# Kernel tuning notes

Measured on AMD Instinct MI355X. Metric: run time of the kernel, lower is better.

The kernel has to match this reference:

```python
import jax, jax.numpy as jnp
import numpy as np

D_MODEL = 1024
N_HEADS = 16
D_K = D_MODEL // N_HEADS
ROPE_THETA = 10000.0


def setup_inputs() -> dict:
    key = jax.random.key(0)
    ks = jax.random.split(key, 5)
    B, S = 2, 2048
    scale = 1.0 / np.sqrt(D_MODEL)
    return {
        "x": jax.random.normal(ks[0], (B, S, D_MODEL), dtype=jnp.float32),
        "token_positions": jnp.arange(S, dtype=jnp.int32),
        "Wq": jax.random.normal(ks[1], (D_MODEL, D_MODEL), dtype=jnp.float32) * scale,
        "Wk": jax.random.normal(ks[2], (D_MODEL, D_MODEL), dtype=jnp.float32) * scale,
        "Wv": jax.random.normal(ks[3], (D_MODEL, D_MODEL), dtype=jnp.float32) * scale,
        "Wo": jax.random.normal(ks[4], (D_MODEL, D_MODEL), dtype=jnp.float32) * scale,
    }


def apply_rope(x, positions):
    # x: [b, h, s, d_k]; interleaved-pair rotary embedding, theta=10000
    half = D_K // 2
    inv_freq = ROPE_THETA ** (-jnp.arange(0, half, dtype=x.dtype) * 2.0 / D_K)  # [half]
    angles = positions.astype(x.dtype)[:, None] * inv_freq[None, :]             # [s, half]
    cos, sin = jnp.cos(angles), jnp.sin(angles)                                 # [s, half]
    x1 = x[..., 0::2]
    x2 = x[..., 1::2]
    r1 = x1 * cos - x2 * sin
    r2 = x1 * sin + x2 * cos
    # re-interleave
    return jnp.stack([r1, r2], axis=-1).reshape(x.shape)


def reference(x, token_positions, Wq, Wk, Wv, Wo):
    B, S, _ = x.shape
    # Linear(d_model, d_model) with no bias: y = x @ W.T
    Q = jnp.einsum("bsd,ed->bse", x, Wq).reshape(B, S, N_HEADS, D_K).transpose(0, 2, 1, 3)
    K = jnp.einsum("bsd,ed->bse", x, Wk).reshape(B, S, N_HEADS, D_K).transpose(0, 2, 1, 3)
    V = jnp.einsum("bsd,ed->bse", x, Wv).reshape(B, S, N_HEADS, D_K).transpose(0, 2, 1, 3)
    Q = apply_rope(Q, token_positions)
    K = apply_rope(K, token_positions)
    scores = jnp.einsum("bhqd,bhkd->bhqk", Q, K) / jnp.sqrt(jnp.asarray(D_K, x.dtype))
    causal = jnp.tril(jnp.ones((S, S), dtype=bool))
    scores = jnp.where(causal[None, None, :, :], scores, jnp.asarray(-jnp.inf, x.dtype))
    attn = jax.nn.softmax(scores, axis=-1)
    out = jnp.einsum("bhqk,bhkd->bhqd", attn, V)            # [b, h, s, d_k]
    out = out.transpose(0, 2, 1, 3).reshape(B, S, D_MODEL)   # [b, s, d_model]
    return jnp.einsum("bsd,ed->bse", out, Wo)
```

## Files before the change

### kernel.cpp

```cpp
#include <hip/hip_runtime.h>
#include <math.h>

#define SEQ 2048
#define NH  16
#define DKH 64
#define DM  1024
#define MR  4096

using bf16x8 = __attribute__((ext_vector_type(8))) short;
using f32x4  = __attribute__((ext_vector_type(4))) float;

__device__ __forceinline__ ushort f2b(float f) {
  unsigned u = __float_as_uint(f);
  return (ushort)((u + 0x7fffu + ((u >> 16) & 1u)) >> 16);
}

__device__ __forceinline__ float exp2_fast(float x) {
  float r; asm("v_exp_f32 %0, %1" : "=v"(r) : "v"(x)); return r;
}

__device__ __forceinline__ unsigned cvt_pk(float lo, float hi) {
  unsigned r; asm("v_cvt_pk_bf16_f32 %0, %1, %2" : "=v"(r) : "v"(lo), "v"(hi));
  return r;
}

__device__ __forceinline__ void gll16(const void* g, void* l) {
  __builtin_amdgcn_global_load_lds(
      (const __attribute__((address_space(1))) void*)g,
      (__attribute__((address_space(3))) void*)l, 16, 0, 0);
}

__global__ __launch_bounds__(256) void cvt_all(
    const float* __restrict__ x,  const float* __restrict__ wq,
    const float* __restrict__ wk, const float* __restrict__ wv,
    const float* __restrict__ wo,
    ushort* __restrict__ xb,  ushort* __restrict__ wqb, ushort* __restrict__ wkb,
    ushort* __restrict__ wvb, ushort* __restrict__ wob)
{
  size_t e = ((size_t)blockIdx.x * 256 + threadIdx.x) * 4;
  const float* s; ushort* d; size_t off;
  if      (e < 4194304) { s = x;  d = xb;  off = e; }
  else if (e < 5242880) { s = wq; d = wqb; off = e - 4194304; }
  else if (e < 6291456) { s = wk; d = wkb; off = e - 5242880; }
  else if (e < 7340032) { s = wv; d = wvb; off = e - 6291456; }
  else                  { s = wo; d = wob; off = e - 7340032; }
  float4 f = *(const float4*)(s + off);
  ushort4 o4 = { f2b(f.x), f2b(f.y), f2b(f.z), f2b(f.w) };
  *(ushort4*)(d + off) = o4;
}

__global__ __launch_bounds__(512) void gemm_qkv(
    const ushort* __restrict__ X,
    const ushort* __restrict__ Wq, const ushort* __restrict__ Wk, const ushort* __restrict__ Wv,
    ushort* __restrict__ Q, ushort* __restrict__ K, ushort* __restrict__ Vt,
    const int* __restrict__ pos)
{
  __shared__ __align__(16) char As[2][16384];
  __shared__ __align__(16) char Bs[2][16384];

  const int id  = blockIdx.x;
  const int xcd = id & 7;
  const int i   = id >> 3;
  const int mt  = xcd * 4 + (i & 3);
  const int nt  = i >> 2;
  const int m0  = mt * 128;
  const int nG  = nt * 128;
  const int z   = nG >> 10;
  const int n0  = nG & 1023;
  const ushort* W = (z == 0) ? Wq : (z == 1) ? Wk : Wv;

  const int tid  = threadIdx.x;
  const int lane = tid & 63;
  const int w    = tid >> 6;
  const int wm   = (w >> 2) * 64;
  const int wn   = (w & 3) * 32;
  const int li   = lane & 15;
  const int g    = lane >> 4;

  f32x4 acc[4][2] = {};

  auto stage = [&](int t, int buf) {
    const int k0 = t * 64;
    #pragma unroll
    for (int it = 0; it < 2; ++it) {
      const int L  = w * 2048 + it * 1024 + lane * 16;
      const int r  = L >> 7;
      const int sc = ((L >> 4) & 7) ^ (r & 7);
      gll16(X + (size_t)(m0 + r) * DM + k0 + sc * 8, &As[buf][w * 2048 + it * 1024]);
      gll16(W + (size_t)(n0 + r) * DM + k0 + sc * 8, &Bs[buf][w * 2048 + it * 1024]);
    }
  };

  auto compute = [&](int buf) {
    #pragma unroll
    for (int ks = 0; ks < 2; ++ks) {
      bf16x8 af[4], bfr[2];
      #pragma unroll
      for (int mf = 0; mf < 4; ++mf) {
        const int row = wm + mf * 16 + li;
        af[mf] = *(const bf16x8*)(&As[buf][row * 128 + (((ks * 4 + g) ^ (row & 7)) << 4)]);
      }
      #pragma unroll
      for (int nf = 0; nf < 2; ++nf) {
        const int row = wn + nf * 16 + li;
        bfr[nf] = *(const bf16x8*)(&Bs[buf][row * 128 + (((ks * 4 + g) ^ (row & 7)) << 4)]);
      }
      #pragma unroll
      for (int mf = 0; mf < 4; ++mf)
        #pragma unroll
        for (int nf = 0; nf < 2; ++nf)
          acc[mf][nf] = __builtin_amdgcn_mfma_f32_16x16x32_bf16(af[mf], bfr[nf], acc[mf][nf], 0, 0, 0);
    }
  };

  stage(0, 0);
  for (int t = 0; t < 16; ++t) {
    if (t < 15) {
      stage(t + 1, (t + 1) & 1);
      __builtin_amdgcn_sched_barrier(0);
      asm volatile("s_waitcnt vmcnt(4)" ::: "memory");
    } else {
      asm volatile("s_waitcnt vmcnt(0)" ::: "memory");
    }
    __builtin_amdgcn_s_barrier();
    __builtin_amdgcn_sched_barrier(0);
    compute(t & 1);
    __builtin_amdgcn_sched_barrier(0);
    __builtin_amdgcn_s_barrier();
  }

  #pragma unroll
  for (int nf = 0; nf < 2; ++nf) {
    const int n = n0 + wn + nf * 16 + li;
    const int h = n >> 6;
    const int d = n & 63;
    if (z == 2) {
      #pragma unroll
      for (int mf = 0; mf < 4; ++mf) {
        const int m  = m0 + wm + mf * 16 + g * 4;
        const int b  = m >> 11;
        const int s2 = m & (SEQ - 1);
        ushort4 pk = { f2b(acc[mf][nf][0]), f2b(acc[mf][nf][1]),
                       f2b(acc[mf][nf][2]), f2b(acc[mf][nf][3]) };
        *(ushort4*)(Vt + (((size_t)b * NH + h) * DKH + d) * SEQ + s2) = pk;
      }
    } else {
      ushort* DST = (z == 0) ? Q : K;
      const float freq = __expf(-(float)(d >> 1) * 0.2878231366242557f);
      #pragma unroll
      for (int mf = 0; mf < 4; ++mf) {
        #pragma unroll
        for (int r = 0; r < 4; ++r) {
          const int m  = m0 + wm + mf * 16 + g * 4 + r;
          const int b  = m >> 11;
          const int s2 = m & (SEQ - 1);
          const float ang = (float)pos[s2] * freq;
          float sn, cs;
          __sincosf(ang, &sn, &cs);
          const float v1 = acc[mf][nf][r];
          const float v2 = __shfl_xor(v1, 1);
          float ov = (d & 1) ? (v2 * sn + v1 * cs)
                             : (v1 * cs - v2 * sn);
          if (z == 0) ov *= 0.1803368801111204f;
          DST[(((size_t)b * NH + h) * SEQ + s2) * DKH + d] = f2b(ov);
        }
      }
    }
  }
}

__global__ __launch_bounds__(512) void gemm_wo(
    const ushort* __restrict__ A, const ushort* __restrict__ W,
    float* __restrict__ out)
{
  __shared__ __align__(16) char As[2][16384];
  __shared__ __align__(16) char Bs[2][16384];

  const int id  = blockIdx.x;
  const int xcd = id & 7;
  const int i   = id >> 3;
  const int mt  = xcd * 4 + (i & 3);
  const int nt  = i >> 2;
  const int m0  = mt * 128;
  const int n0  = nt * 128;

  const int tid  = threadIdx.x;
  const int lane = tid & 63;
  const int w    = tid >> 6;
  const int wm   = (w >> 2) * 64;
  const int wn   = (w & 3) * 32;
  const int li   = lane & 15;
  const int g    = lane >> 4;

  f32x4 acc[4][2] = {};

  auto stage = [&](int t, int buf) {
    const int k0 = t * 64;
    #pragma unroll
    for (int it = 0; it < 2; ++it) {
      const int L  = w * 2048 + it * 1024 + lane * 16;
      const int r  = L >> 7;
      const int sc = ((L >> 4) & 7) ^ (r & 7);
      gll16(A + (size_t)(m0 + r) * DM + k0 + sc * 8, &As[buf][w * 2048 + it * 1024]);
      gll16(W + (size_t)(n0 + r) * DM + k0 + sc * 8, &Bs[buf][w * 2048 + it * 1024]);
    }
  };

  auto compute = [&](int buf) {
    #pragma unroll
    for (int ks = 0; ks < 2; ++ks) {
      bf16x8 af[4], bfr[2];
      #pragma unroll
      for (int mf = 0; mf < 4; ++mf) {
        const int row = wm + mf * 16 + li;
        af[mf] = *(const bf16x8*)(&As[buf][row * 128 + (((ks * 4 + g) ^ (row & 7)) << 4)]);
      }
      #pragma unroll
      for (int nf = 0; nf < 2; ++nf) {
        const int row = wn + nf * 16 + li;
        bfr[nf] = *(const bf16x8*)(&Bs[buf][row * 128 + (((ks * 4 + g) ^ (row & 7)) << 4)]);
      }
      #pragma unroll
      for (int mf = 0; mf < 4; ++mf)
        #pragma unroll
        for (int nf = 0; nf < 2; ++nf)
          acc[mf][nf] = __builtin_amdgcn_mfma_f32_16x16x32_bf16(af[mf], bfr[nf], acc[mf][nf], 0, 0, 0);
    }
  };

  stage(0, 0);
  for (int t = 0; t < 16; ++t) {
    if (t < 15) {
      stage(t + 1, (t + 1) & 1);
      __builtin_amdgcn_sched_barrier(0);
      asm volatile("s_waitcnt vmcnt(4)" ::: "memory");
    } else {
      asm volatile("s_waitcnt vmcnt(0)" ::: "memory");
    }
    __builtin_amdgcn_s_barrier();
    __builtin_amdgcn_sched_barrier(0);
    compute(t & 1);
    __builtin_amdgcn_sched_barrier(0);
    __builtin_amdgcn_s_barrier();
  }

  #pragma unroll
  for (int nf = 0; nf < 2; ++nf)
    #pragma unroll
    for (int mf = 0; mf < 4; ++mf)
      #pragma unroll
      for (int r = 0; r < 4; ++r)
        out[(size_t)(m0 + wm + mf * 16 + g * 4 + r) * DM + n0 + wn + nf * 16 + li] = acc[mf][nf][r];
}

__global__ __launch_bounds__(256) void attn(
    const ushort* __restrict__ Q, const ushort* __restrict__ K,
    const ushort* __restrict__ Vt, ushort* __restrict__ AO)
{
  __shared__ __align__(16) char KsB[2][8192];
  __shared__ __align__(16) char VsB[2][8192];
  __shared__ __align__(16) char Ps[8192];

  const int tid  = threadIdx.x;
  const int lane = tid & 63;
  const int w    = tid >> 6;
  const int li   = lane & 15;
  const int g    = lane >> 4;

  const int bx  = blockIdx.x;
  const int xcd = bx & 7;
  const int idx = bx >> 3;
  const int j   = idx >> 2;
  const int s   = idx & 3;
  const int qb  = (s & 1) ? (31 - j) : j;
  const int bh  = s * 8 + xcd;
  const int q0b = qb * 64;
  const int n   = qb + 1;
  const int q0w = q0b + w * 16;

  const ushort* Qb = Q  + (size_t)bh * SEQ * DKH;
  const ushort* Kb = K  + (size_t)bh * SEQ * DKH;
  const ushort* Vb = Vt + (size_t)bh * DKH * SEQ;
  char* Pw = Ps + w * 2048;

  const bf16x8 qf0 = *(const bf16x8*)(Qb + (size_t)(q0w + li) * DKH + g * 8);
  const bf16x8 qf1 = *(const bf16x8*)(Qb + (size_t)(q0w + li) * DKH + 32 + g * 8);

  f32x4 o[4] = {};
  float m_ = -INFINITY, l_ = 0.f;

  auto stage = [&](int kt, int buf) {
    const int k0 = kt * 64;
    #pragma unroll
    for (int it = 0; it < 2; ++it) {
      const int L  = w * 2048 + it * 1024 + lane * 16;
      const int r  = L >> 7;
      const int sc = ((L >> 4) & 7) ^ (r & 7);
      gll16(Kb + (size_t)(k0 + r) * DKH + sc * 8, &KsB[buf][w * 2048 + it * 1024]);
      gll16(Vb + (size_t)r * SEQ + k0 + sc * 8,   &VsB[buf][w * 2048 + it * 1024]);
    }
  };

  auto computeT = [&](int t, bool diag) {
    const int k0 = t * 64;
    const char* Kc = KsB[t & 1];
    const char* Vc = VsB[t & 1];

    f32x4 st[4] = {};
    __builtin_amdgcn_s_setprio(1);
    #pragma unroll
    for (int nf = 0; nf < 4; ++nf) {
      const int row = nf * 16 + li;
      bf16x8 kfa = *(const bf16x8*)(Kc + row * 128 + (((0 + g) ^ (row & 7)) << 4));
      bf16x8 kfb = *(const bf16x8*)(Kc + row * 128 + (((4 + g) ^ (row & 7)) << 4));
      st[nf] = __builtin_amdgcn_mfma_f32_16x16x32_bf16(kfa, qf0, st[nf], 0, 0, 0);
      st[nf] = __builtin_amdgcn_mfma_f32_16x16x32_bf16(kfb, qf1, st[nf], 0, 0, 0);
    }
    __builtin_amdgcn_s_setprio(0);

    if (diag) {
      #pragma unroll
      for (int nf = 0; nf < 4; ++nf)
        #pragma unroll
        for (int r = 0; r < 4; ++r)
          if (k0 + nf * 16 + g * 4 + r > q0w + li) st[nf][r] = -1e30f;
    }

    float mx = fmaxf(fmaxf(fmaxf(st[0][0], st[0][1]), fmaxf(st[0][2], st[0][3])),
                     fmaxf(fmaxf(st[1][0], st[1][1]), fmaxf(st[1][2], st[1][3])));
    mx = fmaxf(mx, fmaxf(fmaxf(fmaxf(st[2][0], st[2][1]), fmaxf(st[2][2], st[2][3])),
                         fmaxf(fmaxf(st[3][0], st[3][1]), fmaxf(st[3][2], st[3][3]))));
    mx = fmaxf(mx, __shfl_xor(mx, 16));
    mx = fmaxf(mx, __shfl_xor(mx, 32));

    const bool rescale = !__all(mx - m_ <= 8.0f);
    float al = 1.0f;
    if (rescale) {
      const float newm = fmaxf(m_, mx);
      al = exp2_fast(m_ - newm);
      m_ = newm;
    }

    float p[4][4];
    float rs = 0.f;
    #pragma unroll
    for (int nf = 0; nf < 4; ++nf)
      #pragma unroll
      for (int r = 0; r < 4; ++r) {
        p[nf][r] = exp2_fast(st[nf][r] - m_);
        rs += p[nf][r];
      }
    rs += __shfl_xor(rs, 16);
    rs += __shfl_xor(rs, 32);

    if (rescale) {
      l_ = l_ * al + rs;
      float alr[4];
      #pragma unroll
      for (int r = 0; r < 4; ++r) alr[r] = __shfl(al, g * 4 + r);
      #pragma unroll
      for (int nf = 0; nf < 4; ++nf)
        #pragma unroll
        for (int r = 0; r < 4; ++r) o[nf][r] *= alr[r];
    } else {
      l_ += rs;
    }

    #pragma unroll
    for (int nf = 0; nf < 4; ++nf) {
      uint2 pv = { cvt_pk(p[nf][0], p[nf][1]), cvt_pk(p[nf][2], p[nf][3]) };
      const int cw = nf * 2 + (g >> 1);
      *(uint2*)(Pw + li * 128 + ((cw ^ (li & 7)) << 4) + ((g & 1) << 3)) = pv;
    }
    bf16x8 pf0 = *(const bf16x8*)(Pw + li * 128 + (((0 + g) ^ (li & 7)) << 4));
    bf16x8 pf1 = *(const bf16x8*)(Pw + li * 128 + (((4 + g) ^ (li & 7)) << 4));

    __builtin_amdgcn_s_setprio(1);
    #pragma unroll
    for (int nf = 0; nf < 4; ++nf) {
      const int row = nf * 16 + li;
      bf16x8 vfa = *(const bf16x8*)(Vc + row * 128 + (((0 + g) ^ (row & 7)) << 4));
      bf16x8 vfb = *(const bf16x8*)(Vc + row * 128 + (((4 + g) ^ (row & 7)) << 4));
      o[nf] = __builtin_amdgcn_mfma_f32_16x16x32_bf16(pf0, vfa, o[nf], 0, 0, 0);
      o[nf] = __builtin_amdgcn_mfma_f32_16x16x32_bf16(pf1, vfb, o[nf], 0, 0, 0);
    }
    __builtin_amdgcn_s_setprio(0);
  };

  stage(0, 0);
  for (int t = 0; t < n; ++t) {
    if (t + 1 < n) {
      stage(t + 1, (t + 1) & 1);
      __builtin_amdgcn_sched_barrier(0);
      asm volatile("s_waitcnt vmcnt(4)" ::: "memory");
    } else {
      asm volatile("s_waitcnt vmcnt(0)" ::: "memory");
    }
    __builtin_amdgcn_s_barrier();
    __builtin_amdgcn_sched_barrier(0);
    computeT(t, t == n - 1);
    __builtin_amdgcn_sched_barrier(0);
    __builtin_amdgcn_s_barrier();
  }

  const float inv = 1.0f / l_;
  float ir[4];
  #pragma unroll
  for (int r = 0; r < 4; ++r) ir[r] = __shfl(inv, g * 4 + r);

  const int b = bh >> 4, h = bh & 15;
  #pragma unroll
  for (int nf = 0; nf < 4; ++nf)
    #pragma unroll
    for (int r = 0; r < 4; ++r) {
      const int q = q0w + g * 4 + r;
      AO[((size_t)b * SEQ + q) * DM + h * DKH + nf * 16 + li] = f2b(o[nf][r] * ir[r]);
    }
}

extern "C" void kernel_launch(void* const* d_in, const int* in_sizes, int n_in,
                              void* d_out, int out_size, void* d_ws, size_t ws_size,
                              hipStream_t stream)
{
  const float* x   = (const float*)d_in[0];
  const int*   pos = (const int*)  d_in[1];
  const float* Wq  = (const float*)d_in[2];
  const float* Wk  = (const float*)d_in[3];
  const float* Wv  = (const float*)d_in[4];
  const float* Wo  = (const float*)d_in[5];
  float* out = (float*)d_out;

  ushort* ws  = (ushort*)d_ws;
  ushort* xb  = ws;
  ushort* wqb = xb  + 4194304;
  ushort* wkb = wqb + 1048576;
  ushort* wvb = wkb + 1048576;
  ushort* wob = wvb + 1048576;
  ushort* Qb  = wob + 1048576;
  ushort* Kb  = Qb  + 4194304;
  ushort* Vtb = Kb  + 4194304;
  ushort* AOb = Vtb + 4194304;

  cvt_all<<<8192, 256, 0, stream>>>(x, Wq, Wk, Wv, Wo, xb, wqb, wkb, wvb, wob);
  gemm_qkv<<<768, 512, 0, stream>>>(xb, wqb, wkb, wvb, Qb, Kb, Vtb, pos);
  attn<<<1024, 256, 0, stream>>>(Qb, Kb, Vtb, AOb);
  gemm_wo<<<256, 512, 0, stream>>>(AOb, wob, out);
}
```

Measured before the change: 113.6 us.

## Pair complementary causal query blocks per workgroup and stage 128-key tiles

Each attention workgroup now processes two query blocks (p and 31-p) in sequence, so every block does a balanced amount of causal work and the grid halves to 512. K/V staging moves to 128-key chunks double-buffered in larger LDS buffers, giving two 64-key compute steps per barrier pair. This aims to remove load imbalance and tail effects from the triangular work and to cut sync overhead per key. In exchange it uses twice the LDS per block, which may lower occupancy, and it serializes the two segments within one workgroup.

```diff
diff --git a/kernel.cpp b/kernel.cpp
--- a/kernel.cpp
+++ b/kernel.cpp
@@ -257,8 +257,8 @@
     const ushort* __restrict__ Q, const ushort* __restrict__ K,
     const ushort* __restrict__ Vt, ushort* __restrict__ AO)
 {
-  __shared__ __align__(16) char KsB[2][8192];
-  __shared__ __align__(16) char VsB[2][8192];
+  __shared__ __align__(16) char KsB[2][16384];
+  __shared__ __align__(16) char VsB[2][16384];
   __shared__ __align__(16) char Ps[8192];
 
   const int tid  = threadIdx.x;
@@ -270,41 +270,59 @@
   const int bx  = blockIdx.x;
   const int xcd = bx & 7;
   const int idx = bx >> 3;
-  const int j   = idx >> 2;
+  const int p   = idx >> 2;
   const int s   = idx & 3;
-  const int qb  = (s & 1) ? (31 - j) : j;
   const int bh  = s * 8 + xcd;
-  const int q0b = qb * 64;
-  const int n   = qb + 1;
-  const int q0w = q0b + w * 16;
+  const int segA = 31 - p;
+  const int segB = p;
+  const int ncA = (segA + 2) >> 1;
+  const int ncB = (segB + 2) >> 1;
+  const int nT  = ncA + ncB;
 
   const ushort* Qb = Q  + (size_t)bh * SEQ * DKH;
   const ushort* Kb = K  + (size_t)bh * SEQ * DKH;
   const ushort* Vb = Vt + (size_t)bh * DKH * SEQ;
   char* Pw = Ps + w * 2048;
-
-  const bf16x8 qf0 = *(const bf16x8*)(Qb + (size_t)(q0w + li) * DKH + g * 8);
-  const bf16x8 qf1 = *(const bf16x8*)(Qb + (size_t)(q0w + li) * DKH + 32 + g * 8);
+  const int b = bh >> 4, h = bh & 15;
+
+  const int qA = segA * 64 + w * 16;
+  const int qB = segB * 64 + w * 16;
+  const bf16x8 qfA0 = *(const bf16x8*)(Qb + (size_t)(qA + li) * DKH + g * 8);
+  const bf16x8 qfA1 = *(const bf16x8*)(Qb + (size_t)(qA + li) * DKH + 32 + g * 8);
+  const bf16x8 qfB0 = *(const bf16x8*)(Qb + (size_t)(qB + li) * DKH + g * 8);
+  const bf16x8 qfB1 = *(const bf16x8*)(Qb + (size_t)(qB + li) * DKH + 32 + g * 8);
 
   f32x4 o[4] = {};
   float m_ = -INFINITY, l_ = 0.f;
-
-  auto stage = [&](int kt, int buf) {
-    const int k0 = kt * 64;
-    #pragma unroll
-    for (int it = 0; it < 2; ++it) {
-      const int L  = w * 2048 + it * 1024 + lane * 16;
+  bf16x8 qf0 = qfA0, qf1 = qfA1;
+  int seg = segA, q0w = qA;
+
+  auto stage = [&](int i, int buf) {
+    const int c  = (i < ncA) ? i : i - ncA;
+    const int k0 = c * 128;
+    #pragma unroll
+    for (int it = 0; it < 4; ++it) {
+      const int L  = w * 4096 + it * 1024 + lane * 16;
       const int r  = L >> 7;
-      const int sc = ((L >> 4) & 7) ^ (r & 7);
-      gll16(Kb + (size_t)(k0 + r) * DKH + sc * 8, &KsB[buf][w * 2048 + it * 1024]);
-      gll16(Vb + (size_t)r * SEQ + k0 + sc * 8,   &VsB[buf][w * 2048 + it * 1024]);
-    }
-  };
-
-  auto computeT = [&](int t, bool diag) {
+      const int c3 = ((L >> 4) & 7) ^ (r & 7);
+      gll16(Kb + (size_t)(k0 + r) * DKH + c3 * 8, &KsB[buf][w * 4096 + it * 1024]);
+    }
+    #pragma unroll
+    for (int it = 0; it < 4; ++it) {
+      const int L  = w * 4096 + it * 1024 + lane * 16;
+      const int r  = L >> 8;
+      const int lb = L & 255;
+      const int j  = lb >> 7;
+      const int c3 = ((lb >> 4) & 7) ^ (r & 7);
+      gll16(Vb + (size_t)r * SEQ + k0 + j * 64 + c3 * 8, &VsB[buf][w * 4096 + it * 1024]);
+    }
+  };
+
+  auto computeT = [&](int t, int j, int buf) {
     const int k0 = t * 64;
-    const char* Kc = KsB[t & 1];
-    const char* Vc = VsB[t & 1];
+    const char* Kc = &KsB[buf][j * 8192];
+    const char* Vc = &VsB[buf][0];
+    const int vjo = j * 128;
 
     f32x4 st[4] = {};
     __builtin_amdgcn_s_setprio(1);
@@ -318,7 +336,7 @@
     }
     __builtin_amdgcn_s_setprio(0);
 
-    if (diag) {
+    if (t == seg) {
       #pragma unroll
       for (int nf = 0; nf < 4; ++nf)
         #pragma unroll
@@ -341,14 +359,14 @@
       m_ = newm;
     }
 
-    float p[4][4];
+    float pv[4][4];
     float rs = 0.f;
     #pragma unroll
     for (int nf = 0; nf < 4; ++nf)
       #pragma unroll
       for (int r = 0; r < 4; ++r) {
-        p[nf][r] = exp2_fast(st[nf][r] - m_);
-        rs += p[nf][r];
+        pv[nf][r] = exp2_fast(st[nf][r] - m_);
+        rs += pv[nf][r];
       }
     rs += __shfl_xor(rs, 16);
     rs += __shfl_xor(rs, 32);
@@ -368,9 +386,9 @@
 
     #pragma unroll
     for (int nf = 0; nf < 4; ++nf) {
-      uint2 pv = { cvt_pk(p[nf][0], p[nf][1]), cvt_pk(p[nf][2], p[nf][3]) };
+      uint2 pk = { cvt_pk(pv[nf][0], pv[nf][1]), cvt_pk(pv[nf][2], pv[nf][3]) };
       const int cw = nf * 2 + (g >> 1);
-      *(uint2*)(Pw + li * 128 + ((cw ^ (li & 7)) << 4) + ((g & 1) << 3)) = pv;
+      *(uint2*)(Pw + li * 128 + ((cw ^ (li & 7)) << 4) + ((g & 1) << 3)) = pk;
     }
     bf16x8 pf0 = *(const bf16x8*)(Pw + li * 128 + (((0 + g) ^ (li & 7)) << 4));
     bf16x8 pf1 = *(const bf16x8*)(Pw + li * 128 + (((4 + g) ^ (li & 7)) << 4));
@@ -379,43 +397,60 @@
     #pragma unroll
     for (int nf = 0; nf < 4; ++nf) {
       const int row = nf * 16 + li;
-      bf16x8 vfa = *(const bf16x8*)(Vc + row * 128 + (((0 + g) ^ (row & 7)) << 4));
-      bf16x8 vfb = *(const bf16x8*)(Vc + row * 128 + (((4 + g) ^ (row & 7)) << 4));
+      bf16x8 vfa = *(const bf16x8*)(Vc + row * 256 + vjo + (((0 + g) ^ (row & 7)) << 4));
+      bf16x8 vfb = *(const bf16x8*)(Vc + row * 256 + vjo + (((4 + g) ^ (row & 7)) << 4));
       o[nf] = __builtin_amdgcn_mfma_f32_16x16x32_bf16(pf0, vfa, o[nf], 0, 0, 0);
       o[nf] = __builtin_amdgcn_mfma_f32_16x16x32_bf16(pf1, vfb, o[nf], 0, 0, 0);
     }
     __builtin_amdgcn_s_setprio(0);
   };
 
+  auto finalize = [&]() {
+    const float inv = 1.0f / l_;
+    float ir[4];
+    #pragma unroll
+    for (int r = 0; r < 4; ++r) ir[r] = __shfl(inv, g * 4 + r);
+    #pragma unroll
+    for (int nf = 0; nf < 4; ++nf)
+      #pragma unroll
+      for (int r = 0; r < 4; ++r) {
+        const int q = q0w + g * 4 + r;
+        AO[((size_t)b * SEQ + q) * DM + h * DKH + nf * 16 + li] = f2b(o[nf][r] * ir[r]);
+      }
+  };
+
   stage(0, 0);
-  for (int t = 0; t < n; ++t) {
-    if (t + 1 < n) {
-      stage(t + 1, (t + 1) & 1);
+  for (int i = 0; i < nT; ++i) {
+    if (i + 1 < nT) {
+      stage(i + 1, (i + 1) & 1);
       __builtin_amdgcn_sched_barrier(0);
-      asm volatile("s_waitcnt vmcnt(4)" ::: "memory");
+      asm volatile("s_waitcnt vmcnt(8)" ::: "memory");
     } else {
       asm volatile("s_waitcnt vmcnt(0)" ::: "memory");
     }
     __builtin_amdgcn_s_barrier();
     __builtin_amdgcn_sched_barrier(0);
-    computeT(t, t == n - 1);
-    __builtin_amdgcn_sched_barrier(0);
-    __builtin_amdgcn_s_barrier();
+
+    const int c = (i < ncA) ? i : i - ncA;
+    #pragma unroll
+    for (int j = 0; j < 2; ++j) {
+      const int t = 2 * c + j;
+      if (t <= seg) computeT(t, j, i & 1);
+    }
+
+    __builtin_amdgcn_sched_barrier(0);
+    __builtin_amdgcn_s_barrier();
+
+    if (i == ncA - 1) {
+      finalize();
+      #pragma unroll
+      for (int nf = 0; nf < 4; ++nf) o[nf] = f32x4{0.f, 0.f, 0.f, 0.f};
+      m_ = -INFINITY; l_ = 0.f;
+      qf0 = qfB0; qf1 = qfB1;
+      seg = segB; q0w = qB;
+    }
   }
-
-  const float inv = 1.0f / l_;
-  float ir[4];
-  #pragma unroll
-  for (int r = 0; r < 4; ++r) ir[r] = __shfl(inv, g * 4 + r);
-
-  const int b = bh >> 4, h = bh & 15;
-  #pragma unroll
-  for (int nf = 0; nf < 4; ++nf)
-    #pragma unroll
-    for (int r = 0; r < 4; ++r) {
-      const int q = q0w + g * 4 + r;
-      AO[((size_t)b * SEQ + q) * DM + h * DKH + nf * 16 + li] = f2b(o[nf][r] * ir[r]);
-    }
+  finalize();
 }
 
 extern "C" void kernel_launch(void* const* d_in, const int* in_sizes, int n_in,
@@ -443,6 +478,6 @@
 
   cvt_all<<<8192, 256, 0, stream>>>(x, Wq, Wk, Wv, Wo, xb, wqb, wkb, wvb, wob);
   gemm_qkv<<<768, 512, 0, stream>>>(xb, wqb, wkb, wvb, Qb, Kb, Vtb, pos);
-  attn<<<1024, 256, 0, stream>>>(Qb, Kb, Vtb, AOb);
+  attn<<<512, 256, 0, stream>>>(Qb, Kb, Vtb, AOb);
   gemm_wo<<<256, 512, 0, stream>>>(AOb, wob, out);
 }
```

Result: faster. 108.4 us (-4.5%).

## Rewrite attention with 32x32 MFMA, 128-query blocks and register-resident P

Applied to the files above, without the earlier changes.

The attention kernel now gives each block 128 queries, with 32 per wave, and uses 32x32x16 bf16 MFMAs for both QK^T and PV. The P tile is passed to the PV MFMA through permlane32_swap instead of a round trip through shared memory, and the row max and row sum reductions also use permlane swaps. This removes the LDS write/read of P and its shared buffer, halves the grid, and reuses each K/V tile across more queries. In exchange each block does more work, which costs occupancy and load balance. Waves near the diagonal sit idle on some tiles, and the larger f32x16 accumulators raise register pressure.

```diff
diff --git a/kernel.cpp b/kernel.cpp
--- a/kernel.cpp
+++ b/kernel.cpp
@@ -1,4 +1,5 @@
 #include <hip/hip_runtime.h>
+#include <hip/hip_bf16.h>
 #include <math.h>
 
 #define SEQ 2048
@@ -9,6 +10,7 @@
 
 using bf16x8 = __attribute__((ext_vector_type(8))) short;
 using f32x4  = __attribute__((ext_vector_type(4))) float;
+using f32x16 = __attribute__((ext_vector_type(16))) float;
 
 __device__ __forceinline__ ushort f2b(float f) {
   unsigned u = __float_as_uint(f);
@@ -20,8 +22,17 @@
 }
 
 __device__ __forceinline__ unsigned cvt_pk(float lo, float hi) {
-  unsigned r; asm("v_cvt_pk_bf16_f32 %0, %1, %2" : "=v"(r) : "v"(lo), "v"(hi));
-  return r;
+  __hip_bfloat162 h = __float22bfloat162_rn(float2{lo, hi});
+  return *reinterpret_cast<unsigned*>(&h);
+}
+
+__device__ __forceinline__ float xhalf_max(float x) {
+  auto r = __builtin_amdgcn_permlane32_swap(__float_as_uint(x), __float_as_uint(x), false, false);
+  return fmaxf(__uint_as_float(r[0]), __uint_as_float(r[1]));
+}
+__device__ __forceinline__ float xhalf_add(float x) {
+  auto r = __builtin_amdgcn_permlane32_swap(__float_as_uint(x), __float_as_uint(x), false, false);
+  return __uint_as_float(r[0]) + __uint_as_float(r[1]);
 }
 
 __device__ __forceinline__ void gll16(const void* g, void* l) {
@@ -259,34 +270,35 @@
 {
   __shared__ __align__(16) char KsB[2][8192];
   __shared__ __align__(16) char VsB[2][8192];
-  __shared__ __align__(16) char Ps[8192];
 
   const int tid  = threadIdx.x;
   const int lane = tid & 63;
   const int w    = tid >> 6;
-  const int li   = lane & 15;
-  const int g    = lane >> 4;
+  const int lq   = lane & 31;
+  const int hi   = lane >> 5;
 
   const int bx  = blockIdx.x;
   const int xcd = bx & 7;
   const int idx = bx >> 3;
-  const int j   = idx >> 2;
-  const int s   = idx & 3;
-  const int qb  = (s & 1) ? (31 - j) : j;
-  const int bh  = s * 8 + xcd;
-  const int q0b = qb * 64;
-  const int n   = qb + 1;
-  const int q0w = q0b + w * 16;
+  int u, s;
+  if (idx < 32) { u = 15 - (idx >> 1); s = idx & 1; }
+  else          { u = (idx - 32) >> 1; s = 2 + ((idx - 32) & 1); }
+  const int bh   = s * 8 + xcd;
+  const int ntr  = 2 * u + 2;
+  const int q0w  = u * 128 + w * 32;
+  const int q_abs = q0w + lq;
+  const int t_max = (q0w + 31) >> 6;
 
   const ushort* Qb = Q  + (size_t)bh * SEQ * DKH;
   const ushort* Kb = K  + (size_t)bh * SEQ * DKH;
   const ushort* Vb = Vt + (size_t)bh * DKH * SEQ;
-  char* Pw = Ps + w * 2048;
-
-  const bf16x8 qf0 = *(const bf16x8*)(Qb + (size_t)(q0w + li) * DKH + g * 8);
-  const bf16x8 qf1 = *(const bf16x8*)(Qb + (size_t)(q0w + li) * DKH + 32 + g * 8);
-
-  f32x4 o[4] = {};
+
+  bf16x8 qf[4];
+  #pragma unroll
+  for (int db = 0; db < 4; ++db)
+    qf[db] = *(const bf16x8*)(Qb + (size_t)(q0w + lq) * DKH + db * 16 + hi * 8);
+
+  f32x16 o0 = {}, o1 = {};
   float m_ = -INFINITY, l_ = 0.f;
 
   auto stage = [&](int kt, int buf) {
@@ -301,95 +313,85 @@
     }
   };
 
-  auto computeT = [&](int t, bool diag) {
+#define PVSTEP(P, S4) do {                                                   \
+    unsigned A0 = cvt_pk((P)[((S4)&1)*8 + 0], (P)[((S4)&1)*8 + 1]);          \
+    unsigned A1 = cvt_pk((P)[((S4)&1)*8 + 2], (P)[((S4)&1)*8 + 3]);          \
+    unsigned B0 = cvt_pk((P)[((S4)&1)*8 + 4], (P)[((S4)&1)*8 + 5]);          \
+    unsigned B1 = cvt_pk((P)[((S4)&1)*8 + 6], (P)[((S4)&1)*8 + 7]);          \
+    auto r0 = __builtin_amdgcn_permlane32_swap(A0, B0, false, false);        \
+    auto r1 = __builtin_amdgcn_permlane32_swap(A1, B1, false, false);        \
+    int4 ti = { (int)r0[0], (int)r1[0], (int)r0[1], (int)r1[1] };            \
+    bf16x8 pf = *(bf16x8*)&ti;                                               \
+    const int uv = (S4) * 2 + hi;                                            \
+    bf16x8 va = *(const bf16x8*)(Vc + lq * 128      + ((uv ^ (lq & 7)) << 4)); \
+    bf16x8 vb = *(const bf16x8*)(Vc + (32+lq) * 128 + ((uv ^ (lq & 7)) << 4)); \
+    o0 = __builtin_amdgcn_mfma_f32_32x32x16_bf16(va, pf, o0, 0, 0, 0);       \
+    o1 = __builtin_amdgcn_mfma_f32_32x32x16_bf16(vb, pf, o1, 0, 0, 0);       \
+  } while (0)
+
+  auto computeT = [&](int t, int buf, bool diag) {
+    const char* Kc = KsB[buf];
+    const char* Vc = VsB[buf];
     const int k0 = t * 64;
-    const char* Kc = KsB[t & 1];
-    const char* Vc = VsB[t & 1];
-
-    f32x4 st[4] = {};
+
+    f32x16 st0 = {}, st1 = {};
     __builtin_amdgcn_s_setprio(1);
     #pragma unroll
-    for (int nf = 0; nf < 4; ++nf) {
-      const int row = nf * 16 + li;
-      bf16x8 kfa = *(const bf16x8*)(Kc + row * 128 + (((0 + g) ^ (row & 7)) << 4));
-      bf16x8 kfb = *(const bf16x8*)(Kc + row * 128 + (((4 + g) ^ (row & 7)) << 4));
-      st[nf] = __builtin_amdgcn_mfma_f32_16x16x32_bf16(kfa, qf0, st[nf], 0, 0, 0);
-      st[nf] = __builtin_amdgcn_mfma_f32_16x16x32_bf16(kfb, qf1, st[nf], 0, 0, 0);
+    for (int db = 0; db < 4; ++db) {
+      const int uk = db * 2 + hi;
+      bf16x8 ka = *(const bf16x8*)(Kc + lq * 128      + ((uk ^ (lq & 7)) << 4));
+      bf16x8 kb = *(const bf16x8*)(Kc + (32+lq) * 128 + ((uk ^ (lq & 7)) << 4));
+      st0 = __builtin_amdgcn_mfma_f32_32x32x16_bf16(ka, qf[db], st0, 0, 0, 0);
+      st1 = __builtin_amdgcn_mfma_f32_32x32x16_bf16(kb, qf[db], st1, 0, 0, 0);
     }
     __builtin_amdgcn_s_setprio(0);
 
     if (diag) {
       #pragma unroll
-      for (int nf = 0; nf < 4; ++nf)
-        #pragma unroll
-        for (int r = 0; r < 4; ++r)
-          if (k0 + nf * 16 + g * 4 + r > q0w + li) st[nf][r] = -1e30f;
-    }
-
-    float mx = fmaxf(fmaxf(fmaxf(st[0][0], st[0][1]), fmaxf(st[0][2], st[0][3])),
-                     fmaxf(fmaxf(st[1][0], st[1][1]), fmaxf(st[1][2], st[1][3])));
-    mx = fmaxf(mx, fmaxf(fmaxf(fmaxf(st[2][0], st[2][1]), fmaxf(st[2][2], st[2][3])),
-                         fmaxf(fmaxf(st[3][0], st[3][1]), fmaxf(st[3][2], st[3][3]))));
-    mx = fmaxf(mx, __shfl_xor(mx, 16));
-    mx = fmaxf(mx, __shfl_xor(mx, 32));
-
-    const bool rescale = !__all(mx - m_ <= 8.0f);
+      for (int reg = 0; reg < 16; ++reg) {
+        const int kvr = (reg & 3) + 8 * (reg >> 2) + 4 * hi;
+        if (k0 + kvr > q_abs)      st0[reg] = -1e30f;
+        if (k0 + 32 + kvr > q_abs) st1[reg] = -1e30f;
+      }
+    }
+
+    float mx = st0[0];
+    #pragma unroll
+    for (int r = 1; r < 16; ++r) mx = fmaxf(mx, st0[r]);
+    #pragma unroll
+    for (int r = 0; r < 16; ++r) mx = fmaxf(mx, st1[r]);
+    mx = xhalf_max(mx);
+
+    const bool resc = !__all(mx - m_ <= 8.0f);
     float al = 1.0f;
-    if (rescale) {
-      const float newm = fmaxf(m_, mx);
-      al = exp2_fast(m_ - newm);
-      m_ = newm;
-    }
-
-    float p[4][4];
+    if (resc) { const float nm = fmaxf(m_, mx); al = exp2_fast(m_ - nm); m_ = nm; }
+
     float rs = 0.f;
     #pragma unroll
-    for (int nf = 0; nf < 4; ++nf)
-      #pragma unroll
-      for (int r = 0; r < 4; ++r) {
-        p[nf][r] = exp2_fast(st[nf][r] - m_);
-        rs += p[nf][r];
-      }
-    rs += __shfl_xor(rs, 16);
-    rs += __shfl_xor(rs, 32);
-
-    if (rescale) {
+    for (int r = 0; r < 16; ++r) { st0[r] = exp2_fast(st0[r] - m_); rs += st0[r]; }
+    #pragma unroll
+    for (int r = 0; r < 16; ++r) { st1[r] = exp2_fast(st1[r] - m_); rs += st1[r]; }
+    rs = xhalf_add(rs);
+
+    if (resc) {
       l_ = l_ * al + rs;
-      float alr[4];
-      #pragma unroll
-      for (int r = 0; r < 4; ++r) alr[r] = __shfl(al, g * 4 + r);
-      #pragma unroll
-      for (int nf = 0; nf < 4; ++nf)
-        #pragma unroll
-        for (int r = 0; r < 4; ++r) o[nf][r] *= alr[r];
+      #pragma unroll
+      for (int r = 0; r < 16; ++r) { o0[r] *= al; o1[r] *= al; }
     } else {
       l_ += rs;
     }
 
-    #pragma unroll
-    for (int nf = 0; nf < 4; ++nf) {
-      uint2 pv = { cvt_pk(p[nf][0], p[nf][1]), cvt_pk(p[nf][2], p[nf][3]) };
-      const int cw = nf * 2 + (g >> 1);
-      *(uint2*)(Pw + li * 128 + ((cw ^ (li & 7)) << 4) + ((g & 1) << 3)) = pv;
-    }
-    bf16x8 pf0 = *(const bf16x8*)(Pw + li * 128 + (((0 + g) ^ (li & 7)) << 4));
-    bf16x8 pf1 = *(const bf16x8*)(Pw + li * 128 + (((4 + g) ^ (li & 7)) << 4));
-
     __builtin_amdgcn_s_setprio(1);
-    #pragma unroll
-    for (int nf = 0; nf < 4; ++nf) {
-      const int row = nf * 16 + li;
-      bf16x8 vfa = *(const bf16x8*)(Vc + row * 128 + (((0 + g) ^ (row & 7)) << 4));
-      bf16x8 vfb = *(const bf16x8*)(Vc + row * 128 + (((4 + g) ^ (row & 7)) << 4));
-      o[nf] = __builtin_amdgcn_mfma_f32_16x16x32_bf16(pf0, vfa, o[nf], 0, 0, 0);
-      o[nf] = __builtin_amdgcn_mfma_f32_16x16x32_bf16(pf1, vfb, o[nf], 0, 0, 0);
-    }
+    PVSTEP(st0, 0);
+    PVSTEP(st0, 1);
+    PVSTEP(st1, 2);
+    PVSTEP(st1, 3);
     __builtin_amdgcn_s_setprio(0);
   };
 
   stage(0, 0);
-  for (int t = 0; t < n; ++t) {
-    if (t + 1 < n) {
+  for (int t = 0; t < ntr; ++t) {
+    if (t + 1 < ntr) {
       stage(t + 1, (t + 1) & 1);
       __builtin_amdgcn_sched_barrier(0);
       asm volatile("s_waitcnt vmcnt(4)" ::: "memory");
@@ -398,24 +400,27 @@
     }
     __builtin_amdgcn_s_barrier();
     __builtin_amdgcn_sched_barrier(0);
-    computeT(t, t == n - 1);
+    if (t <= t_max) computeT(t, t & 1, t == t_max);
     __builtin_amdgcn_sched_barrier(0);
     __builtin_amdgcn_s_barrier();
   }
 
   const float inv = 1.0f / l_;
-  float ir[4];
-  #pragma unroll
-  for (int r = 0; r < 4; ++r) ir[r] = __shfl(inv, g * 4 + r);
-
   const int b = bh >> 4, h = bh & 15;
-  #pragma unroll
-  for (int nf = 0; nf < 4; ++nf)
-    #pragma unroll
-    for (int r = 0; r < 4; ++r) {
-      const int q = q0w + g * 4 + r;
-      AO[((size_t)b * SEQ + q) * DM + h * DKH + nf * 16 + li] = f2b(o[nf][r] * ir[r]);
-    }
+  ushort* dst = AO + ((size_t)b * SEQ + q_abs) * DM + h * DKH;
+
+#define STORE16(OV, DSUB) do {                                               \
+    _Pragma("unroll")                                                        \
+    for (int rq = 0; rq < 4; ++rq) {                                         \
+      const int d0 = (DSUB) * 32 + rq * 8 + hi * 4;                          \
+      uint2 pk = { cvt_pk((OV)[rq*4+0] * inv, (OV)[rq*4+1] * inv),           \
+                   cvt_pk((OV)[rq*4+2] * inv, (OV)[rq*4+3] * inv) };         \
+      *(uint2*)(dst + d0) = pk;                                              \
+    }                                                                        \
+  } while (0)
+
+  STORE16(o0, 0);
+  STORE16(o1, 1);
 }
 
 extern "C" void kernel_launch(void* const* d_in, const int* in_sizes, int n_in,
@@ -443,6 +448,6 @@
 
   cvt_all<<<8192, 256, 0, stream>>>(x, Wq, Wk, Wv, Wo, xb, wqb, wkb, wvb, wob);
   gemm_qkv<<<768, 512, 0, stream>>>(xb, wqb, wkb, wvb, Qb, Kb, Vtb, pos);
-  attn<<<1024, 256, 0, stream>>>(Qb, Kb, Vtb, AOb);
+  attn<<<512, 256, 0, stream>>>(Qb, Kb, Vtb, AOb);
   gemm_wo<<<256, 512, 0, stream>>>(AOb, wob, out);
 }
```

Result: slower. 118.0 us (+3.8%).

## Drop K/V double buffering in attention and use HIP bf16 pack intrinsic

Applied to the files above, without the earlier changes.

Replaces the double-buffered K/V LDS staging in the attention kernel with a single buffer. Each tile is now loaded and then waited on with __syncthreads before compute, instead of prefetching the next tile with manual vmcnt waits. This cuts LDS use per block from 40KB to 24KB, which may let more blocks share a CU, but global-load latency is no longer overlapped with MFMA work. The inline-asm bf16 pack is also swapped for the __float22bfloat162_rn intrinsic.

```diff
diff --git a/kernel.cpp b/kernel.cpp
--- a/kernel.cpp
+++ b/kernel.cpp
@@ -1,4 +1,5 @@
 #include <hip/hip_runtime.h>
+#include <hip/hip_bf16.h>
 #include <math.h>
 
 #define SEQ 2048
@@ -20,8 +21,8 @@
 }
 
 __device__ __forceinline__ unsigned cvt_pk(float lo, float hi) {
-  unsigned r; asm("v_cvt_pk_bf16_f32 %0, %1, %2" : "=v"(r) : "v"(lo), "v"(hi));
-  return r;
+  __hip_bfloat162 h = __float22bfloat162_rn(float2{lo, hi});
+  return *reinterpret_cast<unsigned*>(&h);
 }
 
 __device__ __forceinline__ void gll16(const void* g, void* l) {
@@ -257,8 +258,8 @@
     const ushort* __restrict__ Q, const ushort* __restrict__ K,
     const ushort* __restrict__ Vt, ushort* __restrict__ AO)
 {
-  __shared__ __align__(16) char KsB[2][8192];
-  __shared__ __align__(16) char VsB[2][8192];
+  __shared__ __align__(16) char Ks[8192];
+  __shared__ __align__(16) char Vs[8192];
   __shared__ __align__(16) char Ps[8192];
 
   const int tid  = threadIdx.x;
@@ -289,30 +290,28 @@
   f32x4 o[4] = {};
   float m_ = -INFINITY, l_ = 0.f;
 
-  auto stage = [&](int kt, int buf) {
+  auto stage = [&](int kt) {
     const int k0 = kt * 64;
     #pragma unroll
     for (int it = 0; it < 2; ++it) {
       const int L  = w * 2048 + it * 1024 + lane * 16;
       const int r  = L >> 7;
       const int sc = ((L >> 4) & 7) ^ (r & 7);
-      gll16(Kb + (size_t)(k0 + r) * DKH + sc * 8, &KsB[buf][w * 2048 + it * 1024]);
-      gll16(Vb + (size_t)r * SEQ + k0 + sc * 8,   &VsB[buf][w * 2048 + it * 1024]);
+      gll16(Kb + (size_t)(k0 + r) * DKH + sc * 8, Ks + w * 2048 + it * 1024);
+      gll16(Vb + (size_t)r * SEQ + k0 + sc * 8,   Vs + w * 2048 + it * 1024);
     }
   };
 
   auto computeT = [&](int t, bool diag) {
     const int k0 = t * 64;
-    const char* Kc = KsB[t & 1];
-    const char* Vc = VsB[t & 1];
 
     f32x4 st[4] = {};
     __builtin_amdgcn_s_setprio(1);
     #pragma unroll
     for (int nf = 0; nf < 4; ++nf) {
       const int row = nf * 16 + li;
-      bf16x8 kfa = *(const bf16x8*)(Kc + row * 128 + (((0 + g) ^ (row & 7)) << 4));
-      bf16x8 kfb = *(const bf16x8*)(Kc + row * 128 + (((4 + g) ^ (row & 7)) << 4));
+      bf16x8 kfa = *(const bf16x8*)(Ks + row * 128 + (((0 + g) ^ (row & 7)) << 4));
+      bf16x8 kfb = *(const bf16x8*)(Ks + row * 128 + (((4 + g) ^ (row & 7)) << 4));
       st[nf] = __builtin_amdgcn_mfma_f32_16x16x32_bf16(kfa, qf0, st[nf], 0, 0, 0);
       st[nf] = __builtin_amdgcn_mfma_f32_16x16x32_bf16(kfb, qf1, st[nf], 0, 0, 0);
     }
@@ -379,28 +378,19 @@
     #pragma unroll
     for (int nf = 0; nf < 4; ++nf) {
       const int row = nf * 16 + li;
-      bf16x8 vfa = *(const bf16x8*)(Vc + row * 128 + (((0 + g) ^ (row & 7)) << 4));
-      bf16x8 vfb = *(const bf16x8*)(Vc + row * 128 + (((4 + g) ^ (row & 7)) << 4));
+      bf16x8 vfa = *(const bf16x8*)(Vs + row * 128 + (((0 + g) ^ (row & 7)) << 4));
+      bf16x8 vfb = *(const bf16x8*)(Vs + row * 128 + (((4 + g) ^ (row & 7)) << 4));
       o[nf] = __builtin_amdgcn_mfma_f32_16x16x32_bf16(pf0, vfa, o[nf], 0, 0, 0);
       o[nf] = __builtin_amdgcn_mfma_f32_16x16x32_bf16(pf1, vfb, o[nf], 0, 0, 0);
     }
     __builtin_amdgcn_s_setprio(0);
   };
 
-  stage(0, 0);
   for (int t = 0; t < n; ++t) {
-    if (t + 1 < n) {
-      stage(t + 1, (t + 1) & 1);
-      __builtin_amdgcn_sched_barrier(0);
-      asm volatile("s_waitcnt vmcnt(4)" ::: "memory");
-    } else {
-      asm volatile("s_waitcnt vmcnt(0)" ::: "memory");
-    }
-    __builtin_amdgcn_s_barrier();
-    __builtin_amdgcn_sched_barrier(0);
+    stage(t);
+    __syncthreads();
     computeT(t, t == n - 1);
-    __builtin_amdgcn_sched_barrier(0);
-    __builtin_amdgcn_s_barrier();
+    __syncthreads();
   }
 
   const float inv = 1.0f / l_;
```

New measurement: 114.6 us. About the same (+0.9%).
